# Performance work log

Hardware: AMD Instinct MI355X
Metric: run time of the kernel (lower is better)

Reference implementation:

```python
import jax, jax.numpy as jnp
import numpy as np

DIM = 512
HID = 4 * DIM
E = 8
B, T = 2, 2048


def setup_inputs() -> dict:
    key = jax.random.key(0)
    ks = jax.random.split(key, 8)
    s = 0.02
    x = jax.random.normal(ks[0], (B, T, DIM), dtype=jnp.float32)
    route = jax.random.randint(ks[1], (B * T,), 0, E, dtype=jnp.int32)
    # stacked per-expert params; Linear y = x @ W + b with W in [in, out] layout
    w_in = jax.random.normal(ks[2], (E, DIM, HID), dtype=jnp.float32) * s
    b_in = jnp.zeros((E, HID), dtype=jnp.float32)
    w_gate = jax.random.normal(ks[3], (E, DIM, HID), dtype=jnp.float32) * s
    b_gate = jnp.zeros((E, HID), dtype=jnp.float32)
    w_out = jax.random.normal(ks[4], (E, HID, DIM), dtype=jnp.float32) * s
    b_out = jnp.zeros((E, DIM), dtype=jnp.float32)
    return {"x": x, "route": route, "w_in": w_in, "b_in": b_in,
            "w_gate": w_gate, "b_gate": b_gate, "w_out": w_out, "b_out": b_out}


def reference(x, route, w_in, b_in, w_gate, b_gate, w_out, b_out):
    Bb, Tt, C = x.shape
    xf = x.reshape(-1, C)  # [N, C]
    out = jnp.zeros_like(xf)
    n_experts = w_in.shape[0]
    # loop over the small fixed expert set; each expert is a SwiGLU FFN,
    # output scattered back by masking (same math as output[idx] += expert(x[idx]))
    for e in range(n_experts):
        mask = (route == e).astype(xf.dtype)[:, None]  # [N, 1]
        h = jax.nn.silu(xf @ w_gate[e] + b_gate[e]) * (xf @ w_in[e] + b_in[e])  # [N, 4C]
        out = out + mask * (h @ w_out[e] + b_out[e])
    return out.reshape(Bb, Tt, C)
```

## Files before the change

kernel.cpp:

```cpp
#include <hip/hip_runtime.h>

#define DIM 512
#define HID 2048
#define NEXP 8

typedef __attribute__((ext_vector_type(8))) short v8s;
typedef __attribute__((ext_vector_type(4))) float v4f;

__device__ __forceinline__ unsigned short f2bf(float f) {
  union { __bf16 b; unsigned short u; } c;
  c.b = (__bf16)f;
  return c.u;
}

__device__ __forceinline__ void gload16(const void* g, void* l) {
  __builtin_amdgcn_global_load_lds(
      (const __attribute__((address_space(1))) unsigned int*)g,
      (__attribute__((address_space(3))) unsigned int*)l, 16, 0, 0);
}

__global__ void route_prep(const int* __restrict__ route, int* __restrict__ meta, int ntok) {
  __shared__ int c[NEXP];
  int t = threadIdx.x;
  if (t < NEXP) c[t] = 0;
  __syncthreads();
  for (int n = t; n < ntok; n += blockDim.x) atomicAdd(&c[route[n]], 1);
  __syncthreads();
  if (t == 0) {
    int acc = 0, pacc = 0;
    for (int e = 0; e < NEXP; ++e) {
      meta[e] = c[e];
      meta[NEXP + e] = acc;
      meta[2 * NEXP + e] = acc;
      meta[3 * NEXP + e] = pacc;
      acc += c[e];
      pacc += ((c[e] + 127) >> 7) << 7;
    }
  }
}

__global__ void fill_perm(const int* __restrict__ route, int* __restrict__ meta,
                          int* __restrict__ perm, int ntok) {
  int n = blockIdx.x * blockDim.x + threadIdx.x;
  if (n < ntok) {
    int p = atomicAdd(&meta[2 * NEXP + route[n]], 1);
    perm[p] = n;
  }
}

__global__ __launch_bounds__(256) void x_conv(
    const float* __restrict__ x, const int* __restrict__ meta,
    const int* __restrict__ perm, unsigned short* __restrict__ xp)
{
  const int bid = blockIdx.x;
  const int e = bid & 7;
  const int mt = bid >> 3;
  const int cnt = meta[e];
  if (mt * 64 >= cnt) return;
  const int off  = meta[NEXP + e];
  const int poff = meta[3 * NEXP + e];
  const int t = threadIdx.x;
  const int r = t & 63, q = t >> 6;
  int arow = mt * 64 + r; if (arow >= cnt) arow = cnt - 1;
  const float* src = x + (size_t)perm[off + arow] * DIM + q * 128;
  unsigned short* dst = xp + (size_t)((poff + mt * 64) >> 6) * 32768;
  #pragma unroll
  for (int j = 0; j < 16; ++j) {
    float4 f0 = ((const float4*)src)[2 * j];
    float4 f1 = ((const float4*)src)[2 * j + 1];
    v8s v;
    v[0] = (short)f2bf(f0.x); v[1] = (short)f2bf(f0.y);
    v[2] = (short)f2bf(f0.z); v[3] = (short)f2bf(f0.w);
    v[4] = (short)f2bf(f1.x); v[5] = (short)f2bf(f1.y);
    v[6] = (short)f2bf(f1.z); v[7] = (short)f2bf(f1.w);
    *(v8s*)(dst + (size_t)((q * 16 + j) * 64 + r) * 8) = v;
  }
}

__global__ __launch_bounds__(256, 3) void gemm1r(
    const unsigned short* __restrict__ xp,
    const float* __restrict__ wg_, const float* __restrict__ bg_,
    const float* __restrict__ wi_, const float* __restrict__ bi_,
    const int* __restrict__ meta,
    unsigned short* __restrict__ hbuf)
{
  const int bid = blockIdx.x;
  const int e = bid & 7;
  const int r_ = bid >> 3;
  const int j = r_ & 15;
  const int mt = r_ >> 4;
  const int cnt = meta[e];
  const int m0 = mt * 64;
  if (m0 >= cnt) return;
  const int poff = meta[3 * NEXP + e];
  const int n0 = j * 128;

  __shared__ __align__(16) unsigned char lds[40960];

  const int t = threadIdx.x;
  const int l = t & 63, w = t >> 6;
  const int wm = w >> 1, wn = w & 1;
  const int fr = l & 15, fg = l >> 4;

  const unsigned short* pa = xp + (size_t)((poff + m0) >> 6) * 32768;
  const float* wg = wg_ + (size_t)e * DIM * HID + n0;
  const float* wi = wi_ + (size_t)e * DIM * HID + n0;

  const int s_kq = t >> 7;
  const int s_n  = t & 127;

  v4f aG[2][4], aI[2][4];
  #pragma unroll
  for (int i = 0; i < 2; ++i)
    #pragma unroll
    for (int q = 0; q < 4; ++q) {
      aG[i][q] = (v4f){0.f, 0.f, 0.f, 0.f};
      aI[i][q] = (v4f){0.f, 0.f, 0.f, 0.f};
    }

  float stG0[8], stG1[8], stI0[8], stI1[8];

  auto wload = [&](int s) {
    const size_t b0 = (size_t)(s * 32 + s_kq * 8) * HID + s_n;
    const size_t b1 = (size_t)(s * 32 + (s_kq + 2) * 8) * HID + s_n;
    #pragma unroll
    for (int q = 0; q < 8; ++q) {
      stG0[q] = wg[b0 + (size_t)q * HID];
      stG1[q] = wg[b1 + (size_t)q * HID];
      stI0[q] = wi[b0 + (size_t)q * HID];
      stI1[q] = wi[b1 + (size_t)q * HID];
    }
  };
  auto wstore = [&](int b) {
    unsigned char* base = lds + b * 20480;
    v8s g0, g1, i0, i1;
    #pragma unroll
    for (int q = 0; q < 8; ++q) {
      g0[q] = (short)f2bf(stG0[q]); g1[q] = (short)f2bf(stG1[q]);
      i0[q] = (short)f2bf(stI0[q]); i1[q] = (short)f2bf(stI1[q]);
    }
    *(v8s*)(base + 4096  + (s_kq * 128 + s_n) * 16)       = g0;
    *(v8s*)(base + 4096  + ((s_kq + 2) * 128 + s_n) * 16) = g1;
    *(v8s*)(base + 12288 + (s_kq * 128 + s_n) * 16)       = i0;
    *(v8s*)(base + 12288 + ((s_kq + 2) * 128 + s_n) * 16) = i1;
  };
  auto aload = [&](int s, int b) {
    gload16(pa + ((size_t)(s * 4 + w) * 64 + l) * 8, lds + b * 20480 + t * 16);
  };

  wload(0);
  aload(0, 0);
  wstore(0);
  __syncthreads();

  int cur = 0;
  for (int s = 0; s < 16; ++s) {
    if (s < 15) { wload(s + 1); aload(s + 1, cur ^ 1); }
    const unsigned char* base = lds + cur * 20480;
    v8s af[2], gf[4], inf[4];
    #pragma unroll
    for (int mf = 0; mf < 2; ++mf)
      af[mf] = *(const v8s*)(base + (fg * 64 + wm * 32 + mf * 16 + fr) * 16);
    #pragma unroll
    for (int nf = 0; nf < 4; ++nf) {
      gf[nf]  = *(const v8s*)(base + 4096  + (fg * 128 + wn * 64 + nf * 16 + fr) * 16);
      inf[nf] = *(const v8s*)(base + 12288 + (fg * 128 + wn * 64 + nf * 16 + fr) * 16);
    }
    #pragma unroll
    for (int mf = 0; mf < 2; ++mf)
      #pragma unroll
      for (int nf = 0; nf < 4; ++nf) {
        aG[mf][nf] = __builtin_amdgcn_mfma_f32_16x16x32_bf16(af[mf], gf[nf],  aG[mf][nf], 0, 0, 0);
        aI[mf][nf] = __builtin_amdgcn_mfma_f32_16x16x32_bf16(af[mf], inf[nf], aI[mf][nf], 0, 0, 0);
      }
    if (s < 15) wstore(cur ^ 1);
    __syncthreads();
    cur ^= 1;
  }

  const size_t tb = (size_t)((poff + m0) >> 6) * 131072;
  #pragma unroll
  for (int nf = 0; nf < 4; ++nf) {
    const int c = n0 + wn * 64 + nf * 16 + fr;
    const float bg = bg_[(size_t)e * HID + c];
    const float bi = bi_[(size_t)e * HID + c];
    #pragma unroll
    for (int mf = 0; mf < 2; ++mf)
      #pragma unroll
      for (int jj = 0; jj < 4; ++jj) {
        const int r = wm * 32 + mf * 16 + fg * 4 + jj;
        const float g = aG[mf][nf][jj] + bg;
        const float v = aI[mf][nf][jj] + bi;
        const float hval = g / (1.f + __expf(-g)) * v;
        hbuf[tb + (size_t)((c >> 3) * 64 + r) * 8 + (c & 7)] = f2bf(hval);
      }
  }
}

__global__ __launch_bounds__(256, 4) void gemm2r(
    const unsigned short* __restrict__ hbuf,
    const float* __restrict__ wo_, const float* __restrict__ bo_,
    const int* __restrict__ meta, const int* __restrict__ perm,
    float* __restrict__ out)
{
  const int bid = blockIdx.x;
  const int e = bid & 7;
  const int r_ = bid >> 3;
  const int jn = r_ & 15;
  const int mt = r_ >> 4;
  const int cnt = meta[e];
  const int m0 = mt * 64;
  if (m0 >= cnt) return;
  const int off = meta[NEXP + e], poff = meta[3 * NEXP + e];
  const int n0 = jn * 32;

  __shared__ __align__(16) unsigned char lds[24576];

  const int t = threadIdx.x;
  const int l = t & 63, w = t >> 6;
  const int wm = w >> 1, wn = w & 1;
  const int fr = l & 15, fg = l >> 4;

  const unsigned short* pa = hbuf + (size_t)((poff + m0) >> 6) * 131072;
  const float* wo = wo_ + (size_t)e * HID * DIM + n0;

  const int b_kq = t >> 5, b_n = t & 31;

  v4f acc[2];
  acc[0] = (v4f){0.f, 0.f, 0.f, 0.f};
  acc[1] = (v4f){0.f, 0.f, 0.f, 0.f};

  float stB[8];
  auto bload = [&](int s) {
    const size_t b0 = (size_t)(s * 64 + b_kq * 8) * DIM + b_n;
    #pragma unroll
    for (int q = 0; q < 8; ++q) stB[q] = wo[b0 + (size_t)q * DIM];
  };
  auto bstore = [&](int b) {
    v8s r;
    #pragma unroll
    for (int q = 0; q < 8; ++q) r[q] = (short)f2bf(stB[q]);
    *(v8s*)(lds + b * 12288 + 8192 + (b_kq * 32 + b_n) * 16) = r;
  };
  auto aload = [&](int s, int b) {
    #pragma unroll
    for (int i = 0; i < 2; ++i)
      gload16(pa + (size_t)s * 4096 + ((size_t)(i * 4 + w) * 64 + l) * 8,
              lds + b * 12288 + ((i * 4 + w) * 64) * 16 + l * 16);
  };

  bload(0);
  aload(0, 0);
  bstore(0);
  __syncthreads();

  int cur = 0;
  for (int s = 0; s < 32; ++s) {
    if (s < 31) { bload(s + 1); aload(s + 1, cur ^ 1); }
    const unsigned char* base = lds + cur * 12288;
    v8s af[2][2], bf[2];
    #pragma unroll
    for (int kk = 0; kk < 2; ++kk) {
      #pragma unroll
      for (int mf = 0; mf < 2; ++mf)
        af[kk][mf] = *(const v8s*)(base + ((kk * 4 + fg) * 64 + wm * 32 + mf * 16 + fr) * 16);
      bf[kk] = *(const v8s*)(base + 8192 + ((kk * 4 + fg) * 32 + wn * 16 + fr) * 16);
    }
    #pragma unroll
    for (int kk = 0; kk < 2; ++kk)
      #pragma unroll
      for (int mf = 0; mf < 2; ++mf)
        acc[mf] = __builtin_amdgcn_mfma_f32_16x16x32_bf16(af[kk][mf], bf[kk], acc[mf], 0, 0, 0);
    if (s < 31) bstore(cur ^ 1);
    __syncthreads();
    cur ^= 1;
  }

  const int c = n0 + wn * 16 + fr;
  const float bo = bo_[(size_t)e * DIM + c];
  #pragma unroll
  for (int mf = 0; mf < 2; ++mf)
    #pragma unroll
    for (int jj = 0; jj < 4; ++jj) {
      const int r = wm * 32 + mf * 16 + fg * 4 + jj;
      if (m0 + r < cnt)
        out[(size_t)perm[off + m0 + r] * DIM + c] = acc[mf][jj] + bo;
    }
}

extern "C" void kernel_launch(void* const* d_in, const int* in_sizes, int n_in,
                              void* d_out, int out_size, void* d_ws, size_t ws_size,
                              hipStream_t stream) {
  const float* x      = (const float*)d_in[0];
  const int*   route  = (const int*)d_in[1];
  const float* w_in   = (const float*)d_in[2];
  const float* b_in   = (const float*)d_in[3];
  const float* w_gate = (const float*)d_in[4];
  const float* b_gate = (const float*)d_in[5];
  const float* w_out  = (const float*)d_in[6];
  const float* b_out  = (const float*)d_in[7];
  float* out = (float*)d_out;

  const int ntok = in_sizes[1];

  int* meta = (int*)d_ws;
  int* perm = (int*)((char*)d_ws + 128);

  unsigned short* xp   = (unsigned short*)((char*)d_ws + 65536);
  unsigned short* hbuf = (unsigned short*)((char*)d_ws + 65536 + 5242880);

  const int MT64 = (ntok + 63) / 64;

  route_prep<<<1, 256, 0, stream>>>(route, meta, ntok);
  fill_perm<<<(ntok + 255) / 256, 256, 0, stream>>>(route, meta, perm, ntok);
  x_conv<<<NEXP * MT64, 256, 0, stream>>>(x, meta, perm, xp);
  gemm1r<<<NEXP * 16 * MT64, 256, 0, stream>>>(
      xp, w_gate, b_gate, w_in, b_in, meta, hbuf);
  gemm2r<<<NEXP * 16 * MT64, 256, 0, stream>>>(
      hbuf, w_out, b_out, meta, perm, out);
}
```

Measured before the change: 110.5 us.

## Deepen weight prefetch to two stages with explicit waitcnt and barriers

Both GEMM kernels now issue the fp32 weight loads two k-steps ahead into registers while the bf16 store to LDS and the activation LDS load happen one step ahead. The plain __syncthreads is replaced by hand-placed s_waitcnt vmcnt/lgkmcnt, raw s_barrier and sched_barrier fences, so the newest weight loads can stay in flight across the barrier. The aim is to hide global-memory latency behind the MFMA work. In exchange the correctness now depends on the hardcoded vmcnt values matching the exact number of outstanding loads, and register pressure goes up.

```diff
diff --git a/kernel.cpp b/kernel.cpp
--- a/kernel.cpp
+++ b/kernel.cpp
@@ -77,7 +77,7 @@
   }
 }
 
-__global__ __launch_bounds__(256, 3) void gemm1r(
+__global__ __launch_bounds__(256, 3) void gemm1p(
     const unsigned short* __restrict__ xp,
     const float* __restrict__ wg_, const float* __restrict__ bg_,
     const float* __restrict__ wi_, const float* __restrict__ bi_,
@@ -149,13 +149,17 @@
   };
 
   wload(0);
+  wstore(0);
   aload(0, 0);
-  wstore(0);
-  __syncthreads();
+  __builtin_amdgcn_sched_barrier(0);
+  wload(1);
+  asm volatile("s_waitcnt vmcnt(32) lgkmcnt(0)" ::: "memory");
+  __builtin_amdgcn_sched_barrier(0);
+  __builtin_amdgcn_s_barrier();
+  __builtin_amdgcn_sched_barrier(0);
 
   int cur = 0;
   for (int s = 0; s < 16; ++s) {
-    if (s < 15) { wload(s + 1); aload(s + 1, cur ^ 1); }
     const unsigned char* base = lds + cur * 20480;
     v8s af[2], gf[4], inf[4];
     #pragma unroll
@@ -173,8 +177,20 @@
         aG[mf][nf] = __builtin_amdgcn_mfma_f32_16x16x32_bf16(af[mf], gf[nf],  aG[mf][nf], 0, 0, 0);
         aI[mf][nf] = __builtin_amdgcn_mfma_f32_16x16x32_bf16(af[mf], inf[nf], aI[mf][nf], 0, 0, 0);
       }
-    if (s < 15) wstore(cur ^ 1);
-    __syncthreads();
+    if (s < 15) {
+      aload(s + 1, cur ^ 1);
+      __builtin_amdgcn_sched_barrier(0);
+      wstore(cur ^ 1);
+      if (s < 14) {
+        wload(s + 2);
+        asm volatile("s_waitcnt vmcnt(32) lgkmcnt(0)" ::: "memory");
+      } else {
+        asm volatile("s_waitcnt vmcnt(0) lgkmcnt(0)" ::: "memory");
+      }
+      __builtin_amdgcn_sched_barrier(0);
+      __builtin_amdgcn_s_barrier();
+      __builtin_amdgcn_sched_barrier(0);
+    }
     cur ^= 1;
   }
 
@@ -197,7 +213,7 @@
   }
 }
 
-__global__ __launch_bounds__(256, 4) void gemm2r(
+__global__ __launch_bounds__(256, 4) void gemm2p(
     const unsigned short* __restrict__ hbuf,
     const float* __restrict__ wo_, const float* __restrict__ bo_,
     const int* __restrict__ meta, const int* __restrict__ perm,
@@ -250,13 +266,17 @@
   };
 
   bload(0);
+  bstore(0);
   aload(0, 0);
-  bstore(0);
-  __syncthreads();
+  __builtin_amdgcn_sched_barrier(0);
+  bload(1);
+  asm volatile("s_waitcnt vmcnt(8) lgkmcnt(0)" ::: "memory");
+  __builtin_amdgcn_sched_barrier(0);
+  __builtin_amdgcn_s_barrier();
+  __builtin_amdgcn_sched_barrier(0);
 
   int cur = 0;
   for (int s = 0; s < 32; ++s) {
-    if (s < 31) { bload(s + 1); aload(s + 1, cur ^ 1); }
     const unsigned char* base = lds + cur * 12288;
     v8s af[2][2], bf[2];
     #pragma unroll
@@ -271,8 +291,20 @@
       #pragma unroll
       for (int mf = 0; mf < 2; ++mf)
         acc[mf] = __builtin_amdgcn_mfma_f32_16x16x32_bf16(af[kk][mf], bf[kk], acc[mf], 0, 0, 0);
-    if (s < 31) bstore(cur ^ 1);
-    __syncthreads();
+    if (s < 31) {
+      aload(s + 1, cur ^ 1);
+      __builtin_amdgcn_sched_barrier(0);
+      bstore(cur ^ 1);
+      if (s < 30) {
+        bload(s + 2);
+        asm volatile("s_waitcnt vmcnt(8) lgkmcnt(0)" ::: "memory");
+      } else {
+        asm volatile("s_waitcnt vmcnt(0) lgkmcnt(0)" ::: "memory");
+      }
+      __builtin_amdgcn_sched_barrier(0);
+      __builtin_amdgcn_s_barrier();
+      __builtin_amdgcn_sched_barrier(0);
+    }
     cur ^= 1;
   }
 
@@ -314,8 +346,8 @@
   route_prep<<<1, 256, 0, stream>>>(route, meta, ntok);
   fill_perm<<<(ntok + 255) / 256, 256, 0, stream>>>(route, meta, perm, ntok);
   x_conv<<<NEXP * MT64, 256, 0, stream>>>(x, meta, perm, xp);
-  gemm1r<<<NEXP * 16 * MT64, 256, 0, stream>>>(
+  gemm1p<<<NEXP * 16 * MT64, 256, 0, stream>>>(
       xp, w_gate, b_gate, w_in, b_in, meta, hbuf);
-  gemm2r<<<NEXP * 16 * MT64, 256, 0, stream>>>(
+  gemm2p<<<NEXP * 16 * MT64, 256, 0, stream>>>(
       hbuf, w_out, b_out, meta, perm, out);
 }
```

Result: slower. 116.4 us (+5.3%).
